# Kernel optimization log

Measured on AMD Instinct MI355X. Metric: run time of the kernel, lower is better.

The kernel has to match this reference:

```python
import jax, jax.numpy as jnp
import numpy as np

H = 16
EPS = 1e-5

def _ln(x, g, b):
    m = jnp.mean(x, -1, keepdims=True)
    v = jnp.mean((x - m) ** 2, -1, keepdims=True)
    return (x - m) * jax.lax.rsqrt(v + EPS) * g + b

def setup_inputs() -> dict:
    key = jax.random.key(0)
    ks = jax.random.split(key, 14)
    B, S, D, F = 2, 2048, 1024, 4096
    s = lambda d: 1.0 / np.sqrt(d)
    return {
        "x": jax.random.normal(ks[0], (B, S, D), jnp.float32),
        "Wqkv": jax.random.normal(ks[1], (D, 3 * D), jnp.float32) * s(D),
        "bqkv": jnp.zeros((3 * D,), jnp.float32),
        "Wo": jax.random.normal(ks[2], (D, D), jnp.float32) * s(D),
        "bo": jnp.zeros((D,), jnp.float32),
        "W1": jax.random.normal(ks[3], (D, F), jnp.float32) * s(D),
        "b1": jnp.zeros((F,), jnp.float32),
        "W2": jax.random.normal(ks[4], (F, D), jnp.float32) * s(F),
        "b2": jnp.zeros((D,), jnp.float32),
        "g1": jnp.ones((D,), jnp.float32),
        "be1": jnp.zeros((D,), jnp.float32),
        "g2": jnp.ones((D,), jnp.float32),
        "be2": jnp.zeros((D,), jnp.float32),
    }

def reference(x, Wqkv, bqkv, Wo, bo, W1, b1, W2, b2, g1, be1, g2, be2):
    B, S, D = x.shape
    hd = D // H
    qkv = x @ Wqkv + bqkv                      # [B,S,3D]
    qkv = qkv.reshape(B, S, H, 3 * hd)         # per-head contiguous q|k|v (matches torch view+chunk)
    q, k, v = jnp.split(qkv, 3, axis=-1)       # each [B,S,H,hd]
    scores = jnp.einsum('bqhd,bkhd->bhqk', q, k) / np.sqrt(hd)
    w = jax.nn.softmax(scores, axis=-1)
    attn = jnp.einsum('bhqk,bkhd->bqhd', w, v).reshape(B, S, D)
    attn = attn @ Wo + bo
    x = _ln(x + attn, g1, be1)
    ff = jax.nn.gelu(x @ W1 + b1, approximate=False) @ W2 + b2
    return _ln(x + ff, g2, be2)
```

## Files before the change

kernel.cpp:

```cpp
#include <hip/hip_runtime.h>
#include <hip/hip_bf16.h>

typedef unsigned int u32;
typedef unsigned short u16;
typedef __attribute__((ext_vector_type(4))) float f32x4;
typedef __attribute__((ext_vector_type(8))) short s16x8;
typedef __attribute__((ext_vector_type(4))) short s16x4;

constexpr int Bb = 2, Ss = 2048, Dd = 1024, Ff = 4096, Hh = 16, HD = 64;
constexpr int Mm = Bb * Ss;

__device__ __forceinline__ u16 f2bf(float f) {
    u32 u = __builtin_bit_cast(u32, f);
    u32 r = (u + 0x7FFFu + ((u >> 16) & 1u)) >> 16;
    return (u16)r;
}
__device__ __forceinline__ float bf2f(u16 b) {
    u32 u = ((u32)b) << 16;
    return __builtin_bit_cast(float, u);
}
__device__ __forceinline__ float gelu_exact(float x) {
    return 0.5f * x * (1.0f + erff(x * 0.70710678118654752f));
}
__device__ __forceinline__ void gload16(const void* g, void* l) {
    __builtin_amdgcn_global_load_lds(
        (const __attribute__((address_space(1))) u32*)g,
        (__attribute__((address_space(3))) u32*)l, 16, 0, 0);
}

template <int BM, int BN, int WM, int WN, bool OUT_BF16, bool GELU>
__global__ __launch_bounds__(WM * WN * 64, (WM * WN == 8) ? 2 : 3)
void gemm_pipe(const u16* __restrict__ A, const u16* __restrict__ Bt,
               const float* __restrict__ bias, void* __restrict__ C,
               int M, int N, int K)
{
    constexpr int NWAVE = WM * WN;
    constexpr int THREADS = NWAVE * 64;
    constexpr int MREP = BM / (WM * 16);
    constexpr int NREP = BN / (WN * 16);
    constexpr int ATILE = BM * 32;
    constexpr int BTILE = BN * 32;
    constexpr int STEP = ATILE + BTILE;
    __shared__ __align__(16) u16 lds[3 * STEP];

    const int tid = threadIdx.x;
    const int l = tid & 63;
    const int w = tid >> 6;
    const int wr = w / WN, wc = w % WN;
    const int brow = blockIdx.y * BM, bcol = blockIdx.x * BN;
    const int nt = K / 32;

    f32x4 acc[MREP][NREP];
#pragma unroll
    for (int i = 0; i < MREP; ++i)
#pragma unroll
        for (int j = 0; j < NREP; ++j) acc[i][j] = (f32x4){0.f, 0.f, 0.f, 0.f};

    const u16* gA[2]; const u16* gB[2];
#pragma unroll
    for (int i = 0; i < 2; ++i) {
        const int flat = i * THREADS + tid;
        const int r = flat >> 2;
        const int lc = (flat & 3) ^ ((r ^ (r >> 2)) & 3);
        gA[i] = A + (size_t)(brow + r) * K + lc * 8;
        gB[i] = Bt + (size_t)(bcol + r) * K + lc * 8;
    }

    int aoff[MREP], boff[NREP];
#pragma unroll
    for (int mi = 0; mi < MREP; ++mi) {
        const int r = wr * (MREP * 16) + mi * 16 + (l & 15);
        aoff[mi] = r * 32 + (((l >> 4) ^ ((r ^ (r >> 2)) & 3)) * 8);
    }
#pragma unroll
    for (int ni = 0; ni < NREP; ++ni) {
        const int r = wc * (NREP * 16) + ni * 16 + (l & 15);
        boff[ni] = r * 32 + (((l >> 4) ^ ((r ^ (r >> 2)) & 3)) * 8);
    }

    auto stage = [&](int s, int t) {
        u16* base = lds + s * STEP;
#pragma unroll
        for (int i = 0; i < 2; ++i)
            gload16(gA[i] + t * 32, base + i * THREADS * 8 + w * 512);
#pragma unroll
        for (int i = 0; i < 2; ++i)
            gload16(gB[i] + t * 32, base + ATILE + i * THREADS * 8 + w * 512);
    };

    stage(0, 0);
    stage(1, 1);
    asm volatile("s_waitcnt vmcnt(4)" ::: "memory");
    __builtin_amdgcn_s_barrier();

    int cur = 0;
    for (int t = 0; t < nt; ++t) {
        if (t + 2 < nt) stage((cur + 2 >= 3) ? cur - 1 : cur + 2, t + 2);

        const u16* Ab = lds + cur * STEP;
        const u16* Bbs = Ab + ATILE;
        s16x8 af[MREP], bfr[NREP];
#pragma unroll
        for (int mi = 0; mi < MREP; ++mi) af[mi] = *(const s16x8*)(Ab + aoff[mi]);
#pragma unroll
        for (int ni = 0; ni < NREP; ++ni) bfr[ni] = *(const s16x8*)(Bbs + boff[ni]);

        __builtin_amdgcn_s_setprio(1);
#pragma unroll
        for (int mi = 0; mi < MREP; ++mi)
#pragma unroll
            for (int ni = 0; ni < NREP; ++ni)
                acc[mi][ni] = __builtin_amdgcn_mfma_f32_16x16x32_bf16(
                    af[mi], bfr[ni], acc[mi][ni], 0, 0, 0);
        __builtin_amdgcn_s_setprio(0);

        if (t + 1 < nt) {
            if (t + 2 < nt) {
                asm volatile("s_waitcnt vmcnt(4)" ::: "memory");
            } else {
                asm volatile("s_waitcnt vmcnt(0)" ::: "memory");
            }
            __builtin_amdgcn_s_barrier();
        }
        cur = (cur + 1 >= 3) ? 0 : cur + 1;
    }

    asm volatile("" ::: "memory");
    float bc[NREP];
#pragma unroll
    for (int ni = 0; ni < NREP; ++ni)
        bc[ni] = bias[bcol + wc * (NREP * 16) + ni * 16 + (l & 15)];
#pragma unroll
    for (int mi = 0; mi < MREP; ++mi) {
        const int row0 = brow + wr * (MREP * 16) + mi * 16 + (l >> 4) * 4;
#pragma unroll
        for (int ni = 0; ni < NREP; ++ni) {
            const int col = bcol + wc * (NREP * 16) + ni * 16 + (l & 15);
#pragma unroll
            for (int rg = 0; rg < 4; ++rg) {
                float v = acc[mi][ni][rg] + bc[ni];
                if (GELU) v = gelu_exact(v);
                if (OUT_BF16)
                    ((u16*)C)[(size_t)(row0 + rg) * N + col] = f2bf(v);
                else
                    ((float*)C)[(size_t)(row0 + rg) * N + col] = v;
            }
        }
    }
}

__global__ __launch_bounds__(256, 4) void attn_mfma(
    const u16* __restrict__ qkv, const u16* __restrict__ Vtg,
    u16* __restrict__ attn)
{
    __shared__ __align__(16) u16 Ks[2][64 * 64];
    __shared__ __align__(16) u16 Vs[2][64 * 64];
    __shared__ __align__(16) u16 Ps[4][16 * 64];
    const int tid = threadIdx.x, l = tid & 63, w = tid >> 6;
    const int qt = blockIdx.x;
    const int bh = blockIdx.y;
    const int b = bh >> 4, h = bh & 15;
    const size_t tokbase = (size_t)b * Ss;
    const int qc = h * 192, kc = qc + 64;

    s16x8 qf[2];
    {
        const int row = qt * 64 + w * 16 + (l & 15);
        const u16* qp = qkv + (tokbase + row) * 3072 + qc + (l >> 4) * 8;
#pragma unroll
        for (int kh = 0; kh < 2; ++kh) {
            s16x8 v = *(const s16x8*)(qp + kh * 32);
#pragma unroll
            for (int j = 0; j < 8; ++j)
                v[j] = (short)f2bf(bf2f((u16)v[j]) * 0.125f);
            qf[kh] = v;
        }
    }

    float mrow[4], lrow[4];
    f32x4 o[4];
#pragma unroll
    for (int rg = 0; rg < 4; ++rg) { mrow[rg] = -1e30f; lrow[rg] = 0.f; }
#pragma unroll
    for (int ni = 0; ni < 4; ++ni) o[ni] = (f32x4){0.f, 0.f, 0.f, 0.f};

    int srow[2], slc[2];
#pragma unroll
    for (int i = 0; i < 2; ++i) {
        const int flat = i * 256 + tid;
        srow[i] = flat >> 3;
        slc[i] = (flat & 7) ^ (srow[i] & 7);
    }
    u16* pw = Ps[w];

    auto stageKV = [&](int s, int kt) {
        const size_t krow = tokbase + kt * 64;
#pragma unroll
        for (int i = 0; i < 2; ++i)
            gload16(qkv + (krow + srow[i]) * 3072 + kc + slc[i] * 8,
                    Ks[s] + i * 2048 + w * 512);
#pragma unroll
        for (int i = 0; i < 2; ++i)
            gload16(Vtg + (size_t)(bh * 64 + srow[i]) * Ss + kt * 64 + slc[i] * 8,
                    Vs[s] + i * 2048 + w * 512);
    };

    stageKV(0, 0);
    __syncthreads();

    for (int kt = 0; kt < Ss / 64; ++kt) {
        const int cur = kt & 1;
        if (kt + 1 < Ss / 64) stageKV(cur ^ 1, kt + 1);

        f32x4 s[4];
#pragma unroll
        for (int ni = 0; ni < 4; ++ni) s[ni] = (f32x4){0.f, 0.f, 0.f, 0.f};
#pragma unroll
        for (int kh = 0; kh < 2; ++kh)
#pragma unroll
            for (int ni = 0; ni < 4; ++ni) {
                const int key = ni * 16 + (l & 15);
                const int ch = (kh * 4 + (l >> 4)) ^ (key & 7);
                s16x8 kf = *(const s16x8*)(Ks[cur] + key * 64 + ch * 8);
                s[ni] = __builtin_amdgcn_mfma_f32_16x16x32_bf16(
                    qf[kh], kf, s[ni], 0, 0, 0);
            }

#pragma unroll
        for (int rg = 0; rg < 4; ++rg) {
            float s0 = s[0][rg], s1 = s[1][rg], s2 = s[2][rg], s3 = s[3][rg];
            float mx = fmaxf(fmaxf(s0, s1), fmaxf(s2, s3));
#pragma unroll
            for (int off = 1; off < 16; off <<= 1)
                mx = fmaxf(mx, __shfl_xor(mx, off, 64));
            const float mnew = fmaxf(mrow[rg], mx);
            const float alpha = __expf(mrow[rg] - mnew);
            float p0 = __expf(s0 - mnew), p1 = __expf(s1 - mnew);
            float p2 = __expf(s2 - mnew), p3 = __expf(s3 - mnew);
            float rs = p0 + p1 + p2 + p3;
#pragma unroll
            for (int off = 1; off < 16; off <<= 1)
                rs += __shfl_xor(rs, off, 64);
            lrow[rg] = lrow[rg] * alpha + rs;
            mrow[rg] = mnew;
#pragma unroll
            for (int ni = 0; ni < 4; ++ni) o[ni][rg] *= alpha;
            const int rq = (l >> 4) * 4 + rg;
            const int kb = l & 15;
            pw[rq * 64 + ((((0 * 16 + kb) >> 3) ^ (rq & 7)) * 8) + (kb & 7)] = f2bf(p0);
            pw[rq * 64 + ((((1 * 16 + kb) >> 3) ^ (rq & 7)) * 8) + (kb & 7)] = f2bf(p1);
            pw[rq * 64 + ((((2 * 16 + kb) >> 3) ^ (rq & 7)) * 8) + (kb & 7)] = f2bf(p2);
            pw[rq * 64 + ((((3 * 16 + kb) >> 3) ^ (rq & 7)) * 8) + (kb & 7)] = f2bf(p3);
        }
        asm volatile("s_waitcnt lgkmcnt(0)" ::: "memory");
        __builtin_amdgcn_sched_barrier(0);

#pragma unroll
        for (int kh = 0; kh < 2; ++kh) {
            const int rq = l & 15;
            const int chp = (kh * 4 + (l >> 4)) ^ (rq & 7);
            s16x8 pf = *(const s16x8*)(pw + rq * 64 + chp * 8);
#pragma unroll
            for (int ni = 0; ni < 4; ++ni) {
                const int d = ni * 16 + (l & 15);
                const int ch = (kh * 4 + (l >> 4)) ^ (d & 7);
                s16x8 vf = *(const s16x8*)(Vs[cur] + d * 64 + ch * 8);
                o[ni] = __builtin_amdgcn_mfma_f32_16x16x32_bf16(
                    pf, vf, o[ni], 0, 0, 0);
            }
        }
        __syncthreads();
    }

#pragma unroll
    for (int rg = 0; rg < 4; ++rg) {
        const float inv = 1.f / lrow[rg];
        const size_t tok = tokbase + qt * 64 + w * 16 + (l >> 4) * 4 + rg;
#pragma unroll
        for (int ni = 0; ni < 4; ++ni)
            attn[tok * Dd + h * 64 + ni * 16 + (l & 15)] =
                f2bf(o[ni][rg] * inv);
    }
}

__global__ __launch_bounds__(256) void conv_bf16(const float* __restrict__ in,
                                                 u16* __restrict__ out) {
    const int i = blockIdx.x * 256 + threadIdx.x;
    float4 v = ((const float4*)in)[i];
    s16x4 o;
    o[0] = (short)f2bf(v.x); o[1] = (short)f2bf(v.y);
    o[2] = (short)f2bf(v.z); o[3] = (short)f2bf(v.w);
    ((s16x4*)out)[i] = o;
}

__global__ __launch_bounds__(256) void transpose_w(const float* __restrict__ W,
                                                   u16* __restrict__ Wt,
                                                   int K, int N) {
    __shared__ u32 tile[64][65];
    const int n0 = blockIdx.x * 64, k0 = blockIdx.y * 64;
    const int t = threadIdx.x;
#pragma unroll
    for (int i = 0; i < 4; ++i) {
        const int flat = i * 256 + t;
        const int kr = flat >> 4, c4 = (flat & 15) * 4;
        float4 v = *(const float4*)(W + (size_t)(k0 + kr) * N + n0 + c4);
        tile[c4 + 0][kr] = (u32)f2bf(v.x);
        tile[c4 + 1][kr] = (u32)f2bf(v.y);
        tile[c4 + 2][kr] = (u32)f2bf(v.z);
        tile[c4 + 3][kr] = (u32)f2bf(v.w);
    }
    __syncthreads();
#pragma unroll
    for (int i = 0; i < 4; ++i) {
        const int flat = i * 256 + t;
        const int nr = flat >> 4, k4 = (flat & 15) * 4;
        s16x4 o;
#pragma unroll
        for (int j = 0; j < 4; ++j) o[j] = (short)tile[nr][k4 + j];
        *(s16x4*)(Wt + (size_t)(n0 + nr) * K + k0 + k4) = o;
    }
}

__global__ __launch_bounds__(256) void vtrans(const u16* __restrict__ qkv,
                                              u16* __restrict__ Vtg) {
    __shared__ u32 tile[64][65];
    const int st = blockIdx.x;
    const int bh = blockIdx.y;
    const int b = bh >> 4, h = bh & 15;
    const int t = threadIdx.x;
    const int vc = h * 192 + 128;
#pragma unroll
    for (int i = 0; i < 4; ++i) {
        const int flat = i * 256 + t;
        const int s = flat >> 4, c4 = (flat & 15) * 4;
        s16x4 v = *(const s16x4*)(qkv + ((size_t)b * Ss + st * 64 + s) * 3072 + vc + c4);
#pragma unroll
        for (int j = 0; j < 4; ++j) tile[c4 + j][s] = (u32)(u16)v[j];
    }
    __syncthreads();
#pragma unroll
    for (int i = 0; i < 4; ++i) {
        const int flat = i * 256 + t;
        const int d = flat >> 4, s4 = (flat & 15) * 4;
        s16x4 o;
#pragma unroll
        for (int j = 0; j < 4; ++j) o[j] = (short)tile[d][s4 + j];
        *(s16x4*)(Vtg + ((size_t)bh * 64 + d) * Ss + st * 64 + s4) = o;
    }
}

template <bool WB>
__global__ __launch_bounds__(256) void ln_res(
    const float* __restrict__ xin, const float* __restrict__ delta,
    const float* __restrict__ g, const float* __restrict__ beta,
    float* __restrict__ out, u16* __restrict__ outb)
{
    __shared__ float red[8];
    const int row = blockIdx.x;
    const int tid = threadIdx.x;
    const size_t ofs = (size_t)row * Dd + tid * 4;

    float4 xv = *(const float4*)(xin + ofs);
    float4 dv = *(const float4*)(delta + ofs);
    float v0 = xv.x + dv.x, v1 = xv.y + dv.y, v2 = xv.z + dv.z, v3 = xv.w + dv.w;

    float sum = v0 + v1 + v2 + v3;
#pragma unroll
    for (int off = 1; off < 64; off <<= 1) sum += __shfl_xor(sum, off, 64);
    const int wid = tid >> 6;
    if ((tid & 63) == 0) red[wid] = sum;
    __syncthreads();
    sum = red[0] + red[1] + red[2] + red[3];
    const float mean = sum * (1.f / Dd);

    float d0 = v0 - mean, d1 = v1 - mean, d2 = v2 - mean, d3 = v3 - mean;
    float s2 = d0 * d0 + d1 * d1 + d2 * d2 + d3 * d3;
#pragma unroll
    for (int off = 1; off < 64; off <<= 1) s2 += __shfl_xor(s2, off, 64);
    if ((tid & 63) == 0) red[4 + wid] = s2;
    __syncthreads();
    s2 = red[4] + red[5] + red[6] + red[7];
    const float rstd = rsqrtf(s2 * (1.f / Dd) + 1e-5f);

    float4 gv = *(const float4*)(g + (size_t)tid * 4);
    float4 bv = *(const float4*)(beta + (size_t)tid * 4);
    float4 ov;
    ov.x = d0 * rstd * gv.x + bv.x;
    ov.y = d1 * rstd * gv.y + bv.y;
    ov.z = d2 * rstd * gv.z + bv.z;
    ov.w = d3 * rstd * gv.w + bv.w;
    *(float4*)(out + ofs) = ov;
    if (WB) {
        s16x4 ob;
        ob[0] = (short)f2bf(ov.x); ob[1] = (short)f2bf(ov.y);
        ob[2] = (short)f2bf(ov.z); ob[3] = (short)f2bf(ov.w);
        *(s16x4*)(outb + ofs) = ob;
    }
}

extern "C" void kernel_launch(void* const* d_in, const int* in_sizes, int n_in,
                              void* d_out, int out_size, void* d_ws, size_t ws_size,
                              hipStream_t stream)
{
    (void)in_sizes; (void)n_in; (void)out_size; (void)ws_size;
    const float* x    = (const float*)d_in[0];
    const float* Wqkv = (const float*)d_in[1];
    const float* bqkv = (const float*)d_in[2];
    const float* Wo   = (const float*)d_in[3];
    const float* bo   = (const float*)d_in[4];
    const float* W1   = (const float*)d_in[5];
    const float* b1   = (const float*)d_in[6];
    const float* W2   = (const float*)d_in[7];
    const float* b2   = (const float*)d_in[8];
    const float* g1   = (const float*)d_in[9];
    const float* be1  = (const float*)d_in[10];
    const float* g2   = (const float*)d_in[11];
    const float* be2  = (const float*)d_in[12];

    char* ws = (char*)d_ws;
    float* x1f   = (float*)(ws + 0);
    u16*   x1b   = (u16*)(ws + 16777216);
    u16*   W1T   = (u16*)(ws + 25165824);
    u16*   W2T   = (u16*)(ws + 33554432);
    u16*   xb    = (u16*)(ws + 41943040);
    u16*   WqkvT = (u16*)(ws + 50331648);
    u16*   WoT   = (u16*)(ws + 56623104);
    u16*   qkv   = (u16*)(ws + 58720256);
    u16*   Vtg   = (u16*)(ws + 83886080);
    u16*   attnB = (u16*)(ws + 92274688);
    float* proj  = (float*)(ws + 58720256);
    u16*   ff1   = (u16*)(ws + 41943040);
    float* tmp2  = (float*)(ws + 75497472);

    dim3 blk(256);

    conv_bf16<<<Mm * Dd / 4 / 256, blk, 0, stream>>>(x, xb);
    transpose_w<<<dim3(3 * Dd / 64, Dd / 64), blk, 0, stream>>>(Wqkv, WqkvT, Dd, 3 * Dd);
    transpose_w<<<dim3(Dd / 64, Dd / 64), blk, 0, stream>>>(Wo, WoT, Dd, Dd);
    transpose_w<<<dim3(Ff / 64, Dd / 64), blk, 0, stream>>>(W1, W1T, Dd, Ff);
    transpose_w<<<dim3(Dd / 64, Ff / 64), blk, 0, stream>>>(W2, W2T, Ff, Dd);

    gemm_pipe<128, 128, 2, 2, true, false>
        <<<dim3(3 * Dd / 128, Mm / 128), blk, 0, stream>>>(
        xb, WqkvT, bqkv, qkv, Mm, 3 * Dd, Dd);

    vtrans<<<dim3(Ss / 64, Bb * Hh), blk, 0, stream>>>(qkv, Vtg);

    attn_mfma<<<dim3(Ss / 64, Bb * Hh), blk, 0, stream>>>(qkv, Vtg, attnB);

    gemm_pipe<128, 128, 2, 2, false, false>
        <<<dim3(Dd / 128, Mm / 128), blk, 0, stream>>>(
        attnB, WoT, bo, proj, Mm, Dd, Dd);

    ln_res<true><<<Mm, blk, 0, stream>>>(x, proj, g1, be1, x1f, x1b);

    gemm_pipe<256, 256, 2, 4, true, true>
        <<<dim3(Ff / 256, Mm / 256), dim3(512), 0, stream>>>(
        x1b, W1T, b1, ff1, Mm, Ff, Dd);

    gemm_pipe<128, 128, 2, 2, false, false>
        <<<dim3(Dd / 128, Mm / 128), blk, 0, stream>>>(
        ff1, W2T, b2, tmp2, Mm, Dd, Ff);

    ln_res<false><<<Mm, blk, 0, stream>>>(x1f, tmp2, g2, be2, (float*)d_out, nullptr);
}
```

Before: 433.1 us.

## Transpose attention MFMA operands so each lane owns one query row

```diff
diff --git a/kernel.cpp b/kernel.cpp
--- a/kernel.cpp
+++ b/kernel.cpp
@@ -6,6 +6,7 @@
 typedef __attribute__((ext_vector_type(4))) float f32x4;
 typedef __attribute__((ext_vector_type(8))) short s16x8;
 typedef __attribute__((ext_vector_type(4))) short s16x4;
+typedef __attribute__((ext_vector_type(2))) unsigned int u32x2;
 
 constexpr int Bb = 2, Ss = 2048, Dd = 1024, Ff = 4096, Hh = 16, HD = 64;
 constexpr int Mm = Bb * Ss;
@@ -18,6 +19,11 @@
 __device__ __forceinline__ float bf2f(u16 b) {
     u32 u = ((u32)b) << 16;
     return __builtin_bit_cast(float, u);
+}
+__device__ __forceinline__ u32 cvtpk_bf16(float lo, float hi) {
+    u32 r;
+    asm("v_cvt_pk_bf16_f32 %0, %1, %2" : "=v"(r) : "v"(lo), "v"(hi));
+    return r;
 }
 __device__ __forceinline__ float gelu_exact(float x) {
     return 0.5f * x * (1.0f + erff(x * 0.70710678118654752f));
@@ -157,6 +163,7 @@
     __shared__ __align__(16) u16 Vs[2][64 * 64];
     __shared__ __align__(16) u16 Ps[4][16 * 64];
     const int tid = threadIdx.x, l = tid & 63, w = tid >> 6;
+    const int q = l & 15, g = l >> 4;
     const int qt = blockIdx.x;
     const int bh = blockIdx.y;
     const int b = bh >> 4, h = bh & 15;
@@ -165,8 +172,8 @@
 
     s16x8 qf[2];
     {
-        const int row = qt * 64 + w * 16 + (l & 15);
-        const u16* qp = qkv + (tokbase + row) * 3072 + qc + (l >> 4) * 8;
+        const int row = qt * 64 + w * 16 + q;
+        const u16* qp = qkv + (tokbase + row) * 3072 + qc + g * 8;
 #pragma unroll
         for (int kh = 0; kh < 2; ++kh) {
             s16x8 v = *(const s16x8*)(qp + kh * 32);
@@ -177,10 +184,8 @@
         }
     }
 
-    float mrow[4], lrow[4];
+    float mrow = -1e30f, lrow = 0.f;
     f32x4 o[4];
-#pragma unroll
-    for (int rg = 0; rg < 4; ++rg) { mrow[rg] = -1e30f; lrow[rg] = 0.f; }
 #pragma unroll
     for (int ni = 0; ni < 4; ++ni) o[ni] = (f32x4){0.f, 0.f, 0.f, 0.f};
 
@@ -193,6 +198,15 @@
     }
     u16* pw = Ps[w];
 
+    int pwr[4];
+#pragma unroll
+    for (int ni = 0; ni < 4; ++ni)
+        pwr[ni] = q * 64 + (((2 * ni + (g >> 1)) ^ (q & 7)) * 8) + (g & 1) * 4;
+    int prd[2];
+#pragma unroll
+    for (int kh = 0; kh < 2; ++kh)
+        prd[kh] = q * 64 + (((kh * 4 + g) ^ (q & 7)) * 8);
+
     auto stageKV = [&](int s, int kt) {
         const size_t krow = tokbase + kt * 64;
 #pragma unroll
@@ -219,67 +233,73 @@
         for (int kh = 0; kh < 2; ++kh)
 #pragma unroll
             for (int ni = 0; ni < 4; ++ni) {
-                const int key = ni * 16 + (l & 15);
-                const int ch = (kh * 4 + (l >> 4)) ^ (key & 7);
+                const int key = ni * 16 + q;
+                const int ch = (kh * 4 + g) ^ (key & 7);
                 s16x8 kf = *(const s16x8*)(Ks[cur] + key * 64 + ch * 8);
                 s[ni] = __builtin_amdgcn_mfma_f32_16x16x32_bf16(
-                    qf[kh], kf, s[ni], 0, 0, 0);
+                    kf, qf[kh], s[ni], 0, 0, 0);
             }
 
-#pragma unroll
-        for (int rg = 0; rg < 4; ++rg) {
-            float s0 = s[0][rg], s1 = s[1][rg], s2 = s[2][rg], s3 = s[3][rg];
-            float mx = fmaxf(fmaxf(s0, s1), fmaxf(s2, s3));
-#pragma unroll
-            for (int off = 1; off < 16; off <<= 1)
-                mx = fmaxf(mx, __shfl_xor(mx, off, 64));
-            const float mnew = fmaxf(mrow[rg], mx);
-            const float alpha = __expf(mrow[rg] - mnew);
-            float p0 = __expf(s0 - mnew), p1 = __expf(s1 - mnew);
-            float p2 = __expf(s2 - mnew), p3 = __expf(s3 - mnew);
-            float rs = p0 + p1 + p2 + p3;
-#pragma unroll
-            for (int off = 1; off < 16; off <<= 1)
-                rs += __shfl_xor(rs, off, 64);
-            lrow[rg] = lrow[rg] * alpha + rs;
-            mrow[rg] = mnew;
-#pragma unroll
-            for (int ni = 0; ni < 4; ++ni) o[ni][rg] *= alpha;
-            const int rq = (l >> 4) * 4 + rg;
-            const int kb = l & 15;
-            pw[rq * 64 + ((((0 * 16 + kb) >> 3) ^ (rq & 7)) * 8) + (kb & 7)] = f2bf(p0);
-            pw[rq * 64 + ((((1 * 16 + kb) >> 3) ^ (rq & 7)) * 8) + (kb & 7)] = f2bf(p1);
-            pw[rq * 64 + ((((2 * 16 + kb) >> 3) ^ (rq & 7)) * 8) + (kb & 7)] = f2bf(p2);
-            pw[rq * 64 + ((((3 * 16 + kb) >> 3) ^ (rq & 7)) * 8) + (kb & 7)] = f2bf(p3);
+        float mx = s[0][0];
+#pragma unroll
+        for (int ni = 0; ni < 4; ++ni)
+#pragma unroll
+            for (int rg = 0; rg < 4; ++rg) mx = fmaxf(mx, s[ni][rg]);
+        mx = fmaxf(mx, __shfl_xor(mx, 16, 64));
+        mx = fmaxf(mx, __shfl_xor(mx, 32, 64));
+        const float mnew = fmaxf(mrow, mx);
+        const float alpha = __expf(mrow - mnew);
+        float p[4][4];
+        float rs = 0.f;
+#pragma unroll
+        for (int ni = 0; ni < 4; ++ni)
+#pragma unroll
+            for (int rg = 0; rg < 4; ++rg) {
+                p[ni][rg] = __expf(s[ni][rg] - mnew);
+                rs += p[ni][rg];
+            }
+        rs += __shfl_xor(rs, 16, 64);
+        rs += __shfl_xor(rs, 32, 64);
+        lrow = lrow * alpha + rs;
+        mrow = mnew;
+#pragma unroll
+        for (int ni = 0; ni < 4; ++ni) {
+            o[ni][0] *= alpha; o[ni][1] *= alpha;
+            o[ni][2] *= alpha; o[ni][3] *= alpha;
+        }
+#pragma unroll
+        for (int ni = 0; ni < 4; ++ni) {
+            u32x2 pkv;
+            pkv[0] = cvtpk_bf16(p[ni][0], p[ni][1]);
+            pkv[1] = cvtpk_bf16(p[ni][2], p[ni][3]);
+            *(u32x2*)(pw + pwr[ni]) = pkv;
         }
         asm volatile("s_waitcnt lgkmcnt(0)" ::: "memory");
         __builtin_amdgcn_sched_barrier(0);
 
 #pragma unroll
         for (int kh = 0; kh < 2; ++kh) {
-            const int rq = l & 15;
-            const int chp = (kh * 4 + (l >> 4)) ^ (rq & 7);
-            s16x8 pf = *(const s16x8*)(pw + rq * 64 + chp * 8);
+            s16x8 pb = *(const s16x8*)(pw + prd[kh]);
 #pragma unroll
             for (int ni = 0; ni < 4; ++ni) {
-                const int d = ni * 16 + (l & 15);
-                const int ch = (kh * 4 + (l >> 4)) ^ (d & 7);
+                const int d = ni * 16 + q;
+                const int ch = (kh * 4 + g) ^ (d & 7);
                 s16x8 vf = *(const s16x8*)(Vs[cur] + d * 64 + ch * 8);
                 o[ni] = __builtin_amdgcn_mfma_f32_16x16x32_bf16(
-                    pf, vf, o[ni], 0, 0, 0);
+                    vf, pb, o[ni], 0, 0, 0);
             }
         }
         __syncthreads();
     }
 
-#pragma unroll
-    for (int rg = 0; rg < 4; ++rg) {
-        const float inv = 1.f / lrow[rg];
-        const size_t tok = tokbase + qt * 64 + w * 16 + (l >> 4) * 4 + rg;
-#pragma unroll
-        for (int ni = 0; ni < 4; ++ni)
-            attn[tok * Dd + h * 64 + ni * 16 + (l & 15)] =
-                f2bf(o[ni][rg] * inv);
+    const float inv = 1.f / lrow;
+    const size_t tok = tokbase + qt * 64 + w * 16 + q;
+#pragma unroll
+    for (int ni = 0; ni < 4; ++ni) {
+        s16x4 ov;
+#pragma unroll
+        for (int rg = 0; rg < 4; ++rg) ov[rg] = (short)f2bf(o[ni][rg] * inv);
+        *(s16x4*)(attn + tok * Dd + h * 64 + ni * 16 + g * 4) = ov;
     }
 }
 
```

New measurement: 376.8 us. -13.0%, faster.
